# Kernel tuning notes

Hardware: AMD Instinct MI355X
Metric: run time of the kernel (lower is better)

The kernel has to match this reference:

```python
import jax, jax.numpy as jnp
import numpy as np
import math

H = 1024      # hidden_size
NH = 16       # num_heads
HD = H // NH  # head_dim
MS = 256      # memory_size
MD = 512      # memory_dim
B, S = 2, 2048


def setup_inputs() -> dict:
    key = jax.random.key(0)
    ks = jax.random.split(key, 12)
    sd = 1.0 / math.sqrt(H)
    inp = {
        "hidden_states": jax.random.normal(ks[0], (B, S, H), dtype=jnp.float32),
        "attention_mask": jnp.zeros((B, S), dtype=jnp.float32),
        "Wq": jax.random.normal(ks[1], (H, H), dtype=jnp.float32) * sd,
        "bq": jnp.zeros((H,), dtype=jnp.float32),
        "Wk": jax.random.normal(ks[2], (H, H), dtype=jnp.float32) * sd,
        "bk": jnp.zeros((H,), dtype=jnp.float32),
        "Wv": jax.random.normal(ks[3], (H, H), dtype=jnp.float32) * sd,
        "bv": jnp.zeros((H,), dtype=jnp.float32),
        "Wo": jax.random.normal(ks[4], (H, H), dtype=jnp.float32) * sd,
        "bo": jnp.zeros((H,), dtype=jnp.float32),
        "memory_values": jax.random.normal(ks[5], (MS, MD), dtype=jnp.float32),
        "Wmp": jax.random.normal(ks[6], (H, MD), dtype=jnp.float32) * (1.0 / math.sqrt(MD)),
        "bmp": jnp.zeros((H,), dtype=jnp.float32),
        "Wma": jax.random.normal(ks[7], (MS, H), dtype=jnp.float32) * sd,
        "bma": jnp.zeros((MS,), dtype=jnp.float32),
    }
    return inp


def reference(hidden_states, attention_mask, Wq, bq, Wk, bk, Wv, bv, Wo, bo,
              memory_values, Wmp, bmp, Wma, bma):
    b, s, h = hidden_states.shape
    scale = math.sqrt(HD)
    # projections (nn.Linear: x @ W.T + b)
    q = hidden_states @ Wq.T + bq
    k = hidden_states @ Wk.T + bk
    v = hidden_states @ Wv.T + bv
    # [b, nh, s, hd]
    q = q.reshape(b, s, NH, HD).transpose(0, 2, 1, 3)
    k = k.reshape(b, s, NH, HD).transpose(0, 2, 1, 3)
    v = v.reshape(b, s, NH, HD).transpose(0, 2, 1, 3)
    # full score matrix [b, nh, s, s] (faithful to original naive MHA)
    attn_scores = jnp.einsum('bhqd,bhkd->bhqk', q, k) / scale
    attn_scores = attn_scores + attention_mask[:, None, None, :] * (-1e9)
    attn_probs = jax.nn.softmax(attn_scores, axis=-1)  # dropout = identity (eval)
    attn_output = jnp.einsum('bhqk,bhkd->bhqd', attn_probs, v)
    attn_output = attn_output.transpose(0, 2, 1, 3).reshape(b, s, h)
    # memory-bank cross attention
    mem_scores = hidden_states @ Wma.T + bma            # [b, s, MS]
    mem_probs = jax.nn.softmax(mem_scores, axis=-1)
    mem_out = mem_probs @ memory_values                  # [b, s, MD]
    mem_out = mem_out @ Wmp.T + bmp                      # [b, s, H]
    combined = attn_output + 0.3 * mem_out
    return combined @ Wo.T + bo
```

## Files before the change

### kernel.cpp

```cpp
#include <hip/hip_runtime.h>

typedef __bf16 bf16;
typedef __bf16 bf16x8 __attribute__((ext_vector_type(8)));
typedef __bf16 bf16x4 __attribute__((ext_vector_type(4)));
typedef float  f32x4  __attribute__((ext_vector_type(4)));
typedef float  f32x16 __attribute__((ext_vector_type(16)));
typedef unsigned u32x2 __attribute__((ext_vector_type(2)));
typedef unsigned u32x4 __attribute__((ext_vector_type(4)));
typedef unsigned long long uptr;

#define MFMA16(a, b, c) __builtin_amdgcn_mfma_f32_16x16x32_bf16((a), (b), (c), 0, 0, 0)
#define MFMA32(a, b, c) __builtin_amdgcn_mfma_f32_32x32x16_bf16((a), (b), (c), 0, 0, 0)

__device__ __forceinline__ void gl_lds16(const void* g, void* l) {
  __builtin_amdgcn_global_load_lds(
      (__attribute__((address_space(1))) void*)(uptr)(g),
      (__attribute__((address_space(3))) void*)(uptr)(l),
      16, 0, 0);
}
__device__ __forceinline__ void gl_lds4(const void* g, void* l) {
  __builtin_amdgcn_global_load_lds(
      (__attribute__((address_space(1))) void*)(uptr)(g),
      (__attribute__((address_space(3))) void*)(uptr)(l),
      4, 0, 0);
}
__device__ __forceinline__ unsigned cvtpk_bf16(float lo, float hi) {
  unsigned r;
  asm("v_cvt_pk_bf16_f32 %0, %1, %2" : "=v"(r) : "v"(lo), "v"(hi));
  return r;
}

__global__ __launch_bounds__(256) void fused_prep(
    const float* __restrict__ X, const float* __restrict__ Wq,
    const float* __restrict__ Wk, const float* __restrict__ Wv,
    const float* __restrict__ Wo, const float* __restrict__ Wma,
    const float* __restrict__ Wmp, const float* __restrict__ mask,
    const float* __restrict__ bq, const float* __restrict__ bk,
    const float* __restrict__ bv, const float* __restrict__ mv,
    bf16* __restrict__ Xb, bf16* __restrict__ Wqkvb, bf16* __restrict__ Wob,
    bf16* __restrict__ Wmab, bf16* __restrict__ Wmpb,
    float* __restrict__ M2, float* __restrict__ bqkv, bf16* __restrict__ mvTb) {
  const int bid = blockIdx.x, t = threadIdx.x;
  auto cvt = [&](const float* src, bf16* dst, int blk) {
    const long i = ((long)blk * 256 + t) * 4;
    const float4 v = *(const float4*)(src + i);
    bf16x4 o = {(bf16)v.x, (bf16)v.y, (bf16)v.z, (bf16)v.w};
    *(bf16x4*)(dst + i) = o;
  };
  if (bid < 4096) cvt(X, Xb, bid);
  else if (bid < 5120) cvt(Wq, Wqkvb, bid - 4096);
  else if (bid < 6144) cvt(Wk, Wqkvb + 1024 * 1024, bid - 5120);
  else if (bid < 7168) cvt(Wv, Wqkvb + 2 * 1024 * 1024, bid - 6144);
  else if (bid < 8192) cvt(Wo, Wob, bid - 7168);
  else if (bid < 8448) cvt(Wma, Wmab, bid - 8192);
  else if (bid < 8960) cvt(Wmp, Wmpb, bid - 8448);
  else if (bid < 8964) {
    const long i = ((long)(bid - 8960) * 256 + t) * 4;
    const float4 v = *(const float4*)(mask + i);
    float4 o = {v.x * -1.44269504e9f, v.y * -1.44269504e9f,
                v.z * -1.44269504e9f, v.w * -1.44269504e9f};
    *(float4*)(M2 + i) = o;
  } else if (bid < 8967) {
    const int s = bid - 8964;
    const float* src = s == 0 ? bq : (s == 1 ? bk : bv);
    *(float4*)(bqkv + s * 1024 + t * 4) = *(const float4*)(src + t * 4);
  } else {
    const int d = bid - 8967;
    mvTb[(long)d * 256 + t] = (bf16)mv[(long)t * 512 + d];
  }
}

__global__ __launch_bounds__(256) void softmax_rows256(const float* __restrict__ in,
                                                       bf16* __restrict__ out) {
  const int w = threadIdx.x >> 6, l = threadIdx.x & 63;
  const long row = (long)blockIdx.x * 4 + w;
  const float4 v = *(const float4*)(in + row * 256 + l * 4);
  float mx = fmaxf(fmaxf(v.x, v.y), fmaxf(v.z, v.w));
  mx = fmaxf(mx, __shfl_xor(mx, 1, 64));
  mx = fmaxf(mx, __shfl_xor(mx, 2, 64));
  mx = fmaxf(mx, __shfl_xor(mx, 4, 64));
  mx = fmaxf(mx, __shfl_xor(mx, 8, 64));
  mx = fmaxf(mx, __shfl_xor(mx, 16, 64));
  mx = fmaxf(mx, __shfl_xor(mx, 32, 64));
  const float e0 = __expf(v.x - mx), e1 = __expf(v.y - mx);
  const float e2 = __expf(v.z - mx), e3 = __expf(v.w - mx);
  float sm = e0 + e1 + e2 + e3;
  sm += __shfl_xor(sm, 1, 64);
  sm += __shfl_xor(sm, 2, 64);
  sm += __shfl_xor(sm, 4, 64);
  sm += __shfl_xor(sm, 8, 64);
  sm += __shfl_xor(sm, 16, 64);
  sm += __shfl_xor(sm, 32, 64);
  const float inv = 1.0f / sm;
  bf16x4 o = {(bf16)(e0 * inv), (bf16)(e1 * inv), (bf16)(e2 * inv), (bf16)(e3 * inv)};
  *(bf16x4*)(out + row * 256 + l * 4) = o;
}

template <typename OutT, bool HAS_ADD>
__global__ __launch_bounds__(256, 3) void gemm_bt(
    const bf16* __restrict__ A, const bf16* __restrict__ B,
    const float* __restrict__ bias, const bf16* __restrict__ addsrc,
    OutT* __restrict__ C, int M, int N, int K, float alpha) {
  __shared__ bf16 lA[2][128 * 64];
  __shared__ bf16 lB[2][64 * 64];
  const int tid = threadIdx.x;
  const int w = tid >> 6, l = tid & 63;
  const int hi = l >> 4, lo = l & 15;
  const int m0 = blockIdx.y * 128, n0 = blockIdx.x * 64;
  const int wm = w * 32;

  const int sr8 = l >> 3;
  const int sc = (l & 7) * 8;
  const long aRow = (long)(m0 + wm + sr8);
  const long bRow = (long)(n0 + w * 16 + sr8);

  auto stage = [&](int p, int k0) {
#pragma unroll
    for (int j = 0; j < 4; ++j)
      gl_lds16(A + (aRow + 8 * j) * K + k0 + sc, (char*)lA[p] + (wm + 8 * j) * 128);
#pragma unroll
    for (int j = 0; j < 2; ++j)
      gl_lds16(B + (bRow + 8 * j) * K + k0 + sc, (char*)lB[p] + (w * 16 + 8 * j) * 128);
  };

  f32x4 acc[2][4] = {};
  stage(0, 0);
  __syncthreads();
  const int nt = K >> 6;

  for (int t = 0; t < nt; ++t) {
    const int p = t & 1;
    if (t + 1 < nt) stage(p ^ 1, (t + 1) << 6);
#pragma unroll
    for (int kk = 0; kk < 2; ++kk) {
      bf16x8 af[2], bfr[4];
#pragma unroll
      for (int mi = 0; mi < 2; ++mi)
        af[mi] = *(const bf16x8*)((const char*)lA[p] + (wm + mi * 16 + lo) * 128 + kk * 64 + hi * 16);
#pragma unroll
      for (int ni = 0; ni < 4; ++ni)
        bfr[ni] = *(const bf16x8*)((const char*)lB[p] + (ni * 16 + lo) * 128 + kk * 64 + hi * 16);
      __builtin_amdgcn_s_setprio(1);
#pragma unroll
      for (int mi = 0; mi < 2; ++mi)
#pragma unroll
        for (int ni = 0; ni < 4; ++ni)
          acc[mi][ni] = MFMA16(af[mi], bfr[ni], acc[mi][ni]);
      __builtin_amdgcn_s_setprio(0);
    }
    __syncthreads();
  }

#pragma unroll
  for (int ni = 0; ni < 4; ++ni) {
    const int col = n0 + ni * 16 + lo;
    const float bv = bias ? bias[col] : 0.0f;
#pragma unroll
    for (int mi = 0; mi < 2; ++mi) {
      const int mrow = m0 + wm + mi * 16 + hi * 4;
#pragma unroll
      for (int r = 0; r < 4; ++r) {
        const long row = mrow + r;
        float v = (acc[mi][ni][r] + bv) * alpha;
        if (HAS_ADD) v += (float)addsrc[row * N + col];
        C[row * (long)N + col] = (OutT)v;
      }
    }
  }
}

__global__ __launch_bounds__(256, 3) void gemm_qkv(
    const bf16* __restrict__ A, const bf16* __restrict__ B,
    const float* __restrict__ bias, bf16* __restrict__ Qo,
    bf16* __restrict__ Ko, bf16* __restrict__ Vto) {
  const int K = 1024;
  __shared__ bf16 lA[128 * 64];
  __shared__ bf16 lB[128 * 64];
  const int tid = threadIdx.x;
  const int w = tid >> 6, l = tid & 63;
  const int hi = l >> 4, lo = l & 15;
  const int m0 = blockIdx.y * 128, n0 = blockIdx.x * 128;
  const int wm = (w >> 1) * 64, wn = (w & 1) * 64;

  const int sr = w * 32 + (l >> 3);
  const int sc = (l & 7) * 8;
  const long aBase = (long)(m0 + sr) * K + sc;
  const long bBase = (long)(n0 + sr) * K + sc;

  f32x4 acc[4][4] = {};

  for (int k0 = 0; k0 < K; k0 += 64) {
#pragma unroll
    for (int j = 0; j < 4; ++j) {
      gl_lds16(A + aBase + (long)8 * j * K + k0, (char*)lA + (w * 32 + 8 * j) * 128);
      gl_lds16(B + bBase + (long)8 * j * K + k0, (char*)lB + (w * 32 + 8 * j) * 128);
    }
    __syncthreads();
#pragma unroll
    for (int kk = 0; kk < 2; ++kk) {
      bf16x8 af[4], bfr[4];
#pragma unroll
      for (int i = 0; i < 4; ++i) {
        af[i]  = *(const bf16x8*)((const char*)lA + (wm + i * 16 + lo) * 128 + kk * 64 + hi * 16);
        bfr[i] = *(const bf16x8*)((const char*)lB + (wn + i * 16 + lo) * 128 + kk * 64 + hi * 16);
      }
#pragma unroll
      for (int mi = 0; mi < 4; ++mi)
#pragma unroll
        for (int ni = 0; ni < 4; ++ni)
          acc[mi][ni] = MFMA16(af[mi], bfr[ni], acc[mi][ni]);
    }
    __syncthreads();
  }

  const int region = n0 >> 10;
#pragma unroll
  for (int ni = 0; ni < 4; ++ni) {
    const int col = n0 + wn + ni * 16 + lo;
    const float bv = bias[col];
#pragma unroll
    for (int mi = 0; mi < 4; ++mi) {
      const int mrow = m0 + wm + mi * 16 + hi * 4;
#pragma unroll
      for (int r = 0; r < 4; ++r) {
        const long row = mrow + r;
        const float v = acc[mi][ni][r] + bv;
        if (region == 0) {
          Qo[row * 1024 + col] = (bf16)v;
        } else if (region == 1) {
          Ko[row * 1024 + (col - 1024)] = (bf16)v;
        } else {
          const long bb = row >> 11, ss = row & 2047;
          Vto[(bb * 1024 + (col - 2048)) * 2048 + ss] = (bf16)v;
        }
      }
    }
  }
}

__global__ __launch_bounds__(256, 4) void attn_fwd(
    const bf16* __restrict__ Q, const bf16* __restrict__ Km,
    const bf16* __restrict__ Vt, const float* __restrict__ M2,
    bf16* __restrict__ Opart, float* __restrict__ ml) {
  __shared__ bf16 lK[2][64 * 64];
  __shared__ bf16 lV[2][64 * 64];
  __shared__ alignas(16) float lM[2][64];
  const int tid = threadIdx.x, w = tid >> 6, l = tid & 63;
  const int q31 = l & 31, h32 = l >> 5;
  const int b = blockIdx.z >> 1, half = blockIdx.z & 1;
  const int hh = blockIdx.y, q0 = blockIdx.x * 128;
  const long S = 2048, H = 1024;
  const int kbase = half * 1024;
  const float SCALE2 = 0.125f * 1.44269504f;

  bf16x8 qf[4];
  const long qrow = (long)b * S + q0 + w * 32 + q31;
#pragma unroll
  for (int sl = 0; sl < 4; ++sl)
    qf[sl] = *(const bf16x8*)(Q + qrow * H + hh * 64 + sl * 16 + h32 * 8);

  f32x16 o0 = {}, o1 = {};
  float mrun = -1e30f, lrun = 0.0f;

  const int swr = w * 16 + (l >> 3);
  const int swc = ((l & 7) ^ (l >> 3)) * 8;

  auto stage = [&](int p, int k0) {
#pragma unroll
    for (int j = 0; j < 2; ++j) {
      gl_lds16(Km + ((long)b * S + k0 + swr + 8 * j) * H + hh * 64 + swc,
               (char*)lK[p] + (w * 16 + 8 * j) * 128);
      gl_lds16(Vt + ((long)b * H + hh * 64 + swr + 8 * j) * S + k0 + swc,
               (char*)lV[p] + (w * 16 + 8 * j) * 128);
    }
    if (w == 0) gl_lds4(M2 + (long)b * S + k0 + l, (char*)lM[p]);
  };

  stage(0, kbase);
  __syncthreads();

  for (int t = 0; t < 16; ++t) {
    const int p = t & 1;
    if (t < 15) stage(p ^ 1, kbase + (t + 1) * 64);

    f32x16 s0 = {}, s1 = {};
    __builtin_amdgcn_s_setprio(1);
#pragma unroll
    for (int sl = 0; sl < 4; ++sl) {
      const int ch = sl * 2 + h32;
      const int cx = (ch ^ (q31 & 7)) * 16;
      const bf16x8 k0f = *(const bf16x8*)((const char*)lK[p] + q31 * 128 + cx);
      const bf16x8 k1f = *(const bf16x8*)((const char*)lK[p] + (32 + q31) * 128 + cx);
      s0 = MFMA32(k0f, qf[sl], s0);
      s1 = MFMA32(k1f, qf[sl], s1);
    }
    __builtin_amdgcn_s_setprio(0);

#pragma unroll
    for (int g = 0; g < 4; ++g) {
      const f32x4 m0 = *(const f32x4*)&lM[p][8 * g + 4 * h32];
      const f32x4 m1 = *(const f32x4*)&lM[p][32 + 8 * g + 4 * h32];
#pragma unroll
      for (int r = 0; r < 4; ++r) {
        s0[4 * g + r] = s0[4 * g + r] * SCALE2 + m0[r];
        s1[4 * g + r] = s1[4 * g + r] * SCALE2 + m1[r];
      }
    }

    f32x16 tm;
#pragma unroll
    for (int i = 0; i < 16; ++i) tm[i] = fmaxf(s0[i], s1[i]);
#pragma unroll
    for (int i = 0; i < 8; ++i) tm[i] = fmaxf(tm[i], tm[i + 8]);
#pragma unroll
    for (int i = 0; i < 4; ++i) tm[i] = fmaxf(tm[i], tm[i + 4]);
    float mx = fmaxf(fmaxf(tm[0], tm[1]), fmaxf(tm[2], tm[3]));
    mx = fmaxf(mx, __shfl_xor(mx, 32, 64));

    if (__any(mx > mrun + 8.0f)) {
      const float mn = fmaxf(mrun, mx);
      const float f = __builtin_amdgcn_exp2f(mrun - mn);
      mrun = mn;
      lrun *= f;
      float fb[16];
#pragma unroll
      for (int reg = 0; reg < 16; ++reg)
        fb[reg] = __shfl(f, (reg & 3) + 8 * (reg >> 2) + 4 * h32, 64);
#pragma unroll
      for (int reg = 0; reg < 16; ++reg) { o0[reg] *= fb[reg]; o1[reg] *= fb[reg]; }
    }

#pragma unroll
    for (int i = 0; i < 16; ++i) s0[i] = __builtin_amdgcn_exp2f(s0[i] - mrun);
#pragma unroll
    for (int i = 0; i < 16; ++i) s1[i] = __builtin_amdgcn_exp2f(s1[i] - mrun);

    f32x16 ts;
#pragma unroll
    for (int i = 0; i < 16; ++i) ts[i] = s0[i] + s1[i];
#pragma unroll
    for (int i = 0; i < 8; ++i) ts[i] += ts[i + 8];
#pragma unroll
    for (int i = 0; i < 4; ++i) ts[i] += ts[i + 4];
    float rs = (ts[0] + ts[1]) + (ts[2] + ts[3]);
    rs += __shfl_xor(rs, 32, 64);
    lrun += rs;

    bf16x8 pa[4];
#pragma unroll
    for (int ks = 0; ks < 4; ++ks) {
      const int rb = (ks & 1) * 8;
      unsigned a0, a1, b0, b1;
      if (ks < 2) {
        a0 = cvtpk_bf16(s0[rb + 0], s0[rb + 1]);
        a1 = cvtpk_bf16(s0[rb + 2], s0[rb + 3]);
        b0 = cvtpk_bf16(s0[rb + 4], s0[rb + 5]);
        b1 = cvtpk_bf16(s0[rb + 6], s0[rb + 7]);
      } else {
        a0 = cvtpk_bf16(s1[rb + 0], s1[rb + 1]);
        a1 = cvtpk_bf16(s1[rb + 2], s1[rb + 3]);
        b0 = cvtpk_bf16(s1[rb + 4], s1[rb + 5]);
        b1 = cvtpk_bf16(s1[rb + 6], s1[rb + 7]);
      }
      const u32x2 r02 = __builtin_amdgcn_permlane32_swap(a0, b0, false, false);
      const u32x2 r13 = __builtin_amdgcn_permlane32_swap(a1, b1, false, false);
      const u32x4 pw = {r02[0], r13[0], r02[1], r13[1]};
      pa[ks] = __builtin_bit_cast(bf16x8, pw);
    }

    __builtin_amdgcn_s_setprio(1);
#pragma unroll
    for (int ks = 0; ks < 4; ++ks) {
      const int ch = ks * 2 + h32;
      const int cx = (ch ^ (q31 & 7)) * 16;
      const bf16x8 v0 = *(const bf16x8*)((const char*)lV[p] + q31 * 128 + cx);
      const bf16x8 v1 = *(const bf16x8*)((const char*)lV[p] + (32 + q31) * 128 + cx);
      o0 = MFMA32(pa[ks], v0, o0);
      o1 = MFMA32(pa[ks], v1, o1);
    }
    __builtin_amdgcn_s_setprio(0);
    __syncthreads();
  }

  if (h32 == 0) {
    float2 v = {mrun, lrun};
    ((float2*)ml)[((long)half * 4096 + (long)b * 2048 + q0 + w * 32 + q31) * 16 + hh] = v;
  }
#pragma unroll
  for (int reg = 0; reg < 16; ++reg) {
    const int row = (reg & 3) + 8 * (reg >> 2) + 4 * h32;
    const long qg = (long)b * 2048 + q0 + w * 32 + row;
    Opart[((long)half * 4096 + qg) * 1024 + hh * 64 + q31]      = (bf16)o0[reg];
    Opart[((long)half * 4096 + qg) * 1024 + hh * 64 + 32 + q31] = (bf16)o1[reg];
  }
}

__global__ __launch_bounds__(256) void attn_combine(
    const bf16* __restrict__ Opart, const float* __restrict__ ml,
    bf16* __restrict__ AO) {
  const long i = ((long)blockIdx.x * 256 + threadIdx.x) * 4;
  const long qg = i >> 10;
  const int h = (int)((i & 1023) >> 6);
  const float2 a = ((const float2*)ml)[qg * 16 + h];
  const float2 c = ((const float2*)ml)[(4096 + qg) * 16 + h];
  const float m = fmaxf(a.x, c.x);
  const float w0 = __builtin_amdgcn_exp2f(a.x - m);
  const float w1 = __builtin_amdgcn_exp2f(c.x - m);
  const float inv = 1.0f / (w0 * a.y + w1 * c.y);
  const bf16x4 O0 = *(const bf16x4*)(Opart + i);
  const bf16x4 O1 = *(const bf16x4*)(Opart + 4096L * 1024 + i);
  bf16x4 o;
#pragma unroll
  for (int j = 0; j < 4; ++j)
    o[j] = (bf16)(((float)O0[j] * w0 + (float)O1[j] * w1) * inv);
  *(bf16x4*)(AO + i) = o;
}

extern "C" void kernel_launch(void* const* d_in, const int* in_sizes, int n_in,
                              void* d_out, int out_size, void* d_ws, size_t ws_size,
                              hipStream_t stream) {
  const float* X    = (const float*)d_in[0];
  const float* mask = (const float*)d_in[1];
  const float* Wq   = (const float*)d_in[2];  const float* bq  = (const float*)d_in[3];
  const float* Wk   = (const float*)d_in[4];  const float* bk  = (const float*)d_in[5];
  const float* Wv   = (const float*)d_in[6];  const float* bv  = (const float*)d_in[7];
  const float* Wo   = (const float*)d_in[8];  const float* bo  = (const float*)d_in[9];
  const float* mv   = (const float*)d_in[10];
  const float* Wmp  = (const float*)d_in[11]; const float* bmp = (const float*)d_in[12];
  const float* Wma  = (const float*)d_in[13]; const float* bma = (const float*)d_in[14];

  char* ws = (char*)d_ws;
  size_t off = 0;
  auto alloc = [&](size_t bytes) -> void* {
    void* p = ws + off;
    off += (bytes + 255) & ~(size_t)255;
    return p;
  };
  const long MS_ = 4096;
  bf16* Xb    = (bf16*)alloc(MS_ * 1024 * 2);
  bf16* Wqkvb = (bf16*)alloc(3072L * 1024 * 2);
  bf16* Wob   = (bf16*)alloc(1024 * 1024 * 2);
  bf16* Wmab  = (bf16*)alloc(256 * 1024 * 2);
  bf16* Wmpb  = (bf16*)alloc(1024 * 512 * 2);
  bf16* mvTb  = (bf16*)alloc(512 * 256 * 2);
  float* M2   = (float*)alloc(MS_ * 4);
  float* bqkv = (float*)alloc(3072 * 4);
  bf16* Qb    = (bf16*)alloc(MS_ * 1024 * 2);
  bf16* Kb    = (bf16*)alloc(MS_ * 1024 * 2);
  bf16* Vtb   = (bf16*)alloc(MS_ * 1024 * 2);
  bf16* AO    = (bf16*)alloc(MS_ * 1024 * 2);
  char* region = (char*)alloc(2 * MS_ * 1024 * 2 + MS_ * 16 * 8 + 1024);
  bf16* Opart = (bf16*)region;
  float* ml   = (float*)(region + 2 * MS_ * 1024 * 2);
  float* MSc  = (float*)region;
  bf16* MP    = (bf16*)(region + MS_ * 256 * 4);
  bf16* MO    = Kb;
  bf16* CB    = Qb;

  fused_prep<<<9479, 256, 0, stream>>>(X, Wq, Wk, Wv, Wo, Wma, Wmp, mask,
                                       bq, bk, bv, mv,
                                       Xb, Wqkvb, Wob, Wmab, Wmpb, M2, bqkv, mvTb);
  gemm_qkv<<<dim3(24, 32), 256, 0, stream>>>(Xb, Wqkvb, bqkv, Qb, Kb, Vtb);
  attn_fwd<<<dim3(16, 16, 4), 256, 0, stream>>>(Qb, Kb, Vtb, M2, Opart, ml);
  attn_combine<<<4096, 256, 0, stream>>>(Opart, ml, AO);
  gemm_bt<float, false><<<dim3(4, 32), 256, 0, stream>>>(Xb, Wmab, bma, nullptr, MSc, 4096, 256, 1024, 1.0f);
  softmax_rows256<<<1024, 256, 0, stream>>>(MSc, MP);
  gemm_bt<bf16, false><<<dim3(8, 32), 256, 0, stream>>>(MP, mvTb, nullptr, nullptr, MO, 4096, 512, 256, 1.0f);
  gemm_bt<bf16, true><<<dim3(16, 32), 256, 0, stream>>>(MO, Wmpb, bmp, AO, CB, 4096, 1024, 512, 0.3f);
  gemm_bt<float, false><<<dim3(16, 32), 256, 0, stream>>>(CB, Wob, bo, nullptr, (float*)d_out, 4096, 1024, 1024, 1.0f);
}
```

Baseline: 163.8 us.

## Fold memory projection into output weights and split attention keys into quarters

Precomputes Wo·(0.3·Wmp) as extra weight columns and a merged bias, so the memory projection GEMM with its residual add is dropped. The attention output and memory output are concatenated along K into one 1536-wide buffer for a single final GEMM. Attention is split into four key quarters with a remapped 1D grid and a higher occupancy target, the mask is read directly from global memory instead of LDS, and the combine step merges four partials. This adds a small weight-only GEMM, a per-call weight transpose, and an extra rounding of the folded weights to bf16.

```diff
diff --git a/kernel.cpp b/kernel.cpp
--- a/kernel.cpp
+++ b/kernel.cpp
@@ -18,12 +18,6 @@
       (__attribute__((address_space(3))) void*)(uptr)(l),
       16, 0, 0);
 }
-__device__ __forceinline__ void gl_lds4(const void* g, void* l) {
-  __builtin_amdgcn_global_load_lds(
-      (__attribute__((address_space(1))) void*)(uptr)(g),
-      (__attribute__((address_space(3))) void*)(uptr)(l),
-      4, 0, 0);
-}
 __device__ __forceinline__ unsigned cvtpk_bf16(float lo, float hi) {
   unsigned r;
   asm("v_cvt_pk_bf16_f32 %0, %1, %2" : "=v"(r) : "v"(lo), "v"(hi));
@@ -37,9 +31,11 @@
     const float* __restrict__ Wmp, const float* __restrict__ mask,
     const float* __restrict__ bq, const float* __restrict__ bk,
     const float* __restrict__ bv, const float* __restrict__ mv,
-    bf16* __restrict__ Xb, bf16* __restrict__ Wqkvb, bf16* __restrict__ Wob,
-    bf16* __restrict__ Wmab, bf16* __restrict__ Wmpb,
-    float* __restrict__ M2, float* __restrict__ bqkv, bf16* __restrict__ mvTb) {
+    const float* __restrict__ bo, const float* __restrict__ bmp,
+    bf16* __restrict__ Xb, bf16* __restrict__ Wqkvb, bf16* __restrict__ WCAT,
+    bf16* __restrict__ Wmab, bf16* __restrict__ WmpT,
+    float* __restrict__ M2, float* __restrict__ bqkv, bf16* __restrict__ mvTb,
+    float* __restrict__ bmix) {
   const int bid = blockIdx.x, t = threadIdx.x;
   auto cvt = [&](const float* src, bf16* dst, int blk) {
     const long i = ((long)blk * 256 + t) * 4;
@@ -51,10 +47,21 @@
   else if (bid < 5120) cvt(Wq, Wqkvb, bid - 4096);
   else if (bid < 6144) cvt(Wk, Wqkvb + 1024 * 1024, bid - 5120);
   else if (bid < 7168) cvt(Wv, Wqkvb + 2 * 1024 * 1024, bid - 6144);
-  else if (bid < 8192) cvt(Wo, Wob, bid - 7168);
-  else if (bid < 8448) cvt(Wma, Wmab, bid - 8192);
-  else if (bid < 8960) cvt(Wmp, Wmpb, bid - 8448);
-  else if (bid < 8964) {
+  else if (bid < 8192) {
+    const long i = ((long)(bid - 7168) * 256 + t) * 4;
+    const long row = i >> 10, col = i & 1023;
+    const float4 v = *(const float4*)(Wo + i);
+    bf16x4 o = {(bf16)v.x, (bf16)v.y, (bf16)v.z, (bf16)v.w};
+    *(bf16x4*)(WCAT + row * 1536 + col) = o;
+  } else if (bid < 8448) cvt(Wma, Wmab, bid - 8192);
+  else if (bid < 8960) {
+    const int m = bid - 8448;
+#pragma unroll
+    for (int j = 0; j < 4; ++j) {
+      const int k = t * 4 + j;
+      WmpT[(long)m * 1024 + k] = (bf16)Wmp[(long)k * 512 + m];
+    }
+  } else if (bid < 8964) {
     const long i = ((long)(bid - 8960) * 256 + t) * 4;
     const float4 v = *(const float4*)(mask + i);
     float4 o = {v.x * -1.44269504e9f, v.y * -1.44269504e9f,
@@ -64,9 +71,18 @@
     const int s = bid - 8964;
     const float* src = s == 0 ? bq : (s == 1 ? bk : bv);
     *(float4*)(bqkv + s * 1024 + t * 4) = *(const float4*)(src + t * 4);
-  } else {
+  } else if (bid < 9479) {
     const int d = bid - 8967;
     mvTb[(long)d * 256 + t] = (bf16)mv[(long)t * 512 + d];
+  } else {
+    const int n = (bid - 9479) * 256 + t;
+    float acc = 0.0f;
+    for (int k4 = 0; k4 < 256; ++k4) {
+      const float4 wv = *(const float4*)(Wo + (long)n * 1024 + k4 * 4);
+      const float4 bb = *(const float4*)(bmp + k4 * 4);
+      acc += wv.x * bb.x + wv.y * bb.y + wv.z * bb.z + wv.w * bb.w;
+    }
+    bmix[n] = bo[n] + 0.3f * acc;
   }
 }
 
@@ -96,11 +112,11 @@
   *(bf16x4*)(out + row * 256 + l * 4) = o;
 }
 
-template <typename OutT, bool HAS_ADD>
+template <typename OutT>
 __global__ __launch_bounds__(256, 3) void gemm_bt(
     const bf16* __restrict__ A, const bf16* __restrict__ B,
-    const float* __restrict__ bias, const bf16* __restrict__ addsrc,
-    OutT* __restrict__ C, int M, int N, int K, float alpha) {
+    const float* __restrict__ bias, OutT* __restrict__ C,
+    int M, int N, int K, int lda, int ldc, float alpha) {
   __shared__ bf16 lA[2][128 * 64];
   __shared__ bf16 lB[2][64 * 64];
   const int tid = threadIdx.x;
@@ -117,7 +133,7 @@
   auto stage = [&](int p, int k0) {
 #pragma unroll
     for (int j = 0; j < 4; ++j)
-      gl_lds16(A + (aRow + 8 * j) * K + k0 + sc, (char*)lA[p] + (wm + 8 * j) * 128);
+      gl_lds16(A + (aRow + 8 * j) * lda + k0 + sc, (char*)lA[p] + (wm + 8 * j) * 128);
 #pragma unroll
     for (int j = 0; j < 2; ++j)
       gl_lds16(B + (bRow + 8 * j) * K + k0 + sc, (char*)lB[p] + (w * 16 + 8 * j) * 128);
@@ -161,9 +177,7 @@
 #pragma unroll
       for (int r = 0; r < 4; ++r) {
         const long row = mrow + r;
-        float v = (acc[mi][ni][r] + bv) * alpha;
-        if (HAS_ADD) v += (float)addsrc[row * N + col];
-        C[row * (long)N + col] = (OutT)v;
+        C[row * (long)ldc + col] = (OutT)((acc[mi][ni][r] + bv) * alpha);
       }
     }
   }
@@ -238,19 +252,20 @@
   }
 }
 
-__global__ __launch_bounds__(256, 4) void attn_fwd(
+__global__ __launch_bounds__(256, 8) void attn_fwd(
     const bf16* __restrict__ Q, const bf16* __restrict__ Km,
     const bf16* __restrict__ Vt, const float* __restrict__ M2,
     bf16* __restrict__ Opart, float* __restrict__ ml) {
   __shared__ bf16 lK[2][64 * 64];
   __shared__ bf16 lV[2][64 * 64];
-  __shared__ alignas(16) float lM[2][64];
+  const int lin = blockIdx.x;
+  const int role = ((lin & 7) << 8) | (lin >> 3);
+  const int qt = role & 15, hh = (role >> 4) & 15, zz = role >> 8;
+  const int b = zz >> 2, quarter = zz & 3;
+  const int q0 = qt * 128, kbase = quarter * 512;
   const int tid = threadIdx.x, w = tid >> 6, l = tid & 63;
   const int q31 = l & 31, h32 = l >> 5;
-  const int b = blockIdx.z >> 1, half = blockIdx.z & 1;
-  const int hh = blockIdx.y, q0 = blockIdx.x * 128;
   const long S = 2048, H = 1024;
-  const int kbase = half * 1024;
   const float SCALE2 = 0.125f * 1.44269504f;
 
   bf16x8 qf[4];
@@ -273,15 +288,21 @@
       gl_lds16(Vt + ((long)b * H + hh * 64 + swr + 8 * j) * S + k0 + swc,
                (char*)lV[p] + (w * 16 + 8 * j) * 128);
     }
-    if (w == 0) gl_lds4(M2 + (long)b * S + k0 + l, (char*)lM[p]);
   };
 
   stage(0, kbase);
   __syncthreads();
 
-  for (int t = 0; t < 16; ++t) {
-    const int p = t & 1;
-    if (t < 15) stage(p ^ 1, kbase + (t + 1) * 64);
+  for (int t = 0; t < 8; ++t) {
+    const int p = t & 1, k0 = kbase + t * 64;
+    if (t < 7) stage(p ^ 1, k0 + 64);
+
+    f32x4 mk0[4], mk1[4];
+#pragma unroll
+    for (int g = 0; g < 4; ++g) {
+      mk0[g] = *(const f32x4*)(M2 + (long)b * S + k0 + 8 * g + 4 * h32);
+      mk1[g] = *(const f32x4*)(M2 + (long)b * S + k0 + 32 + 8 * g + 4 * h32);
+    }
 
     f32x16 s0 = {}, s1 = {};
     __builtin_amdgcn_s_setprio(1);
@@ -297,15 +318,12 @@
     __builtin_amdgcn_s_setprio(0);
 
 #pragma unroll
-    for (int g = 0; g < 4; ++g) {
-      const f32x4 m0 = *(const f32x4*)&lM[p][8 * g + 4 * h32];
-      const f32x4 m1 = *(const f32x4*)&lM[p][32 + 8 * g + 4 * h32];
+    for (int g = 0; g < 4; ++g)
 #pragma unroll
       for (int r = 0; r < 4; ++r) {
-        s0[4 * g + r] = s0[4 * g + r] * SCALE2 + m0[r];
-        s1[4 * g + r] = s1[4 * g + r] * SCALE2 + m1[r];
+        s0[4 * g + r] = s0[4 * g + r] * SCALE2 + mk0[g][r];
+        s1[4 * g + r] = s1[4 * g + r] * SCALE2 + mk1[g][r];
       }
-    }
 
     f32x16 tm;
 #pragma unroll
@@ -384,36 +402,43 @@
 
   if (h32 == 0) {
     float2 v = {mrun, lrun};
-    ((float2*)ml)[((long)half * 4096 + (long)b * 2048 + q0 + w * 32 + q31) * 16 + hh] = v;
+    ((float2*)ml)[((long)quarter * 4096 + (long)b * 2048 + q0 + w * 32 + q31) * 16 + hh] = v;
   }
 #pragma unroll
   for (int reg = 0; reg < 16; ++reg) {
     const int row = (reg & 3) + 8 * (reg >> 2) + 4 * h32;
     const long qg = (long)b * 2048 + q0 + w * 32 + row;
-    Opart[((long)half * 4096 + qg) * 1024 + hh * 64 + q31]      = (bf16)o0[reg];
-    Opart[((long)half * 4096 + qg) * 1024 + hh * 64 + 32 + q31] = (bf16)o1[reg];
+    Opart[((long)quarter * 4096 + qg) * 1024 + hh * 64 + q31]      = (bf16)o0[reg];
+    Opart[((long)quarter * 4096 + qg) * 1024 + hh * 64 + 32 + q31] = (bf16)o1[reg];
   }
 }
 
 __global__ __launch_bounds__(256) void attn_combine(
     const bf16* __restrict__ Opart, const float* __restrict__ ml,
-    bf16* __restrict__ AO) {
+    bf16* __restrict__ CAT) {
   const long i = ((long)blockIdx.x * 256 + threadIdx.x) * 4;
   const long qg = i >> 10;
   const int h = (int)((i & 1023) >> 6);
-  const float2 a = ((const float2*)ml)[qg * 16 + h];
-  const float2 c = ((const float2*)ml)[(4096 + qg) * 16 + h];
-  const float m = fmaxf(a.x, c.x);
-  const float w0 = __builtin_amdgcn_exp2f(a.x - m);
-  const float w1 = __builtin_amdgcn_exp2f(c.x - m);
-  const float inv = 1.0f / (w0 * a.y + w1 * c.y);
-  const bf16x4 O0 = *(const bf16x4*)(Opart + i);
-  const bf16x4 O1 = *(const bf16x4*)(Opart + 4096L * 1024 + i);
+  float2 a[4];
+#pragma unroll
+  for (int j = 0; j < 4; ++j) a[j] = ((const float2*)ml)[((long)j * 4096 + qg) * 16 + h];
+  const float m = fmaxf(fmaxf(a[0].x, a[1].x), fmaxf(a[2].x, a[3].x));
+  float wgt[4], den = 0.0f;
+#pragma unroll
+  for (int j = 0; j < 4; ++j) { wgt[j] = __builtin_amdgcn_exp2f(a[j].x - m); den += wgt[j] * a[j].y; }
+  const float inv = 1.0f / den;
+  float acc[4] = {};
+#pragma unroll
+  for (int j = 0; j < 4; ++j) {
+    const bf16x4 O = *(const bf16x4*)(Opart + (long)j * 4096 * 1024 + i);
+#pragma unroll
+    for (int e = 0; e < 4; ++e) acc[e] += (float)O[e] * wgt[j];
+  }
+  const long row = i >> 10, col = i & 1023;
   bf16x4 o;
 #pragma unroll
-  for (int j = 0; j < 4; ++j)
-    o[j] = (bf16)(((float)O0[j] * w0 + (float)O1[j] * w1) * inv);
-  *(bf16x4*)(AO + i) = o;
+  for (int e = 0; e < 4; ++e) o[e] = (bf16)(acc[e] * inv);
+  *(bf16x4*)(CAT + row * 1536 + col) = o;
 }
 
 extern "C" void kernel_launch(void* const* d_in, const int* in_sizes, int n_in,
@@ -439,33 +464,36 @@
   const long MS_ = 4096;
   bf16* Xb    = (bf16*)alloc(MS_ * 1024 * 2);
   bf16* Wqkvb = (bf16*)alloc(3072L * 1024 * 2);
-  bf16* Wob   = (bf16*)alloc(1024 * 1024 * 2);
+  bf16* WCAT  = (bf16*)alloc(1024L * 1536 * 2);
   bf16* Wmab  = (bf16*)alloc(256 * 1024 * 2);
-  bf16* Wmpb  = (bf16*)alloc(1024 * 512 * 2);
+  bf16* WmpT  = (bf16*)alloc(512L * 1024 * 2);
   bf16* mvTb  = (bf16*)alloc(512 * 256 * 2);
   float* M2   = (float*)alloc(MS_ * 4);
   float* bqkv = (float*)alloc(3072 * 4);
+  float* bmix = (float*)alloc(1024 * 4);
   bf16* Qb    = (bf16*)alloc(MS_ * 1024 * 2);
   bf16* Kb    = (bf16*)alloc(MS_ * 1024 * 2);
   bf16* Vtb   = (bf16*)alloc(MS_ * 1024 * 2);
-  bf16* AO    = (bf16*)alloc(MS_ * 1024 * 2);
-  char* region = (char*)alloc(2 * MS_ * 1024 * 2 + MS_ * 16 * 8 + 1024);
+  bf16* CAT   = (bf16*)alloc(MS_ * 1536 * 2);
+  char* region = (char*)alloc(4 * MS_ * 1024 * 2 + 4 * MS_ * 16 * 8 + 1024);
   bf16* Opart = (bf16*)region;
-  float* ml   = (float*)(region + 2 * MS_ * 1024 * 2);
+  float* ml   = (float*)(region + 4 * MS_ * 1024 * 2);
   float* MSc  = (float*)region;
   bf16* MP    = (bf16*)(region + MS_ * 256 * 4);
-  bf16* MO    = Kb;
-  bf16* CB    = Qb;
-
-  fused_prep<<<9479, 256, 0, stream>>>(X, Wq, Wk, Wv, Wo, Wma, Wmp, mask,
-                                       bq, bk, bv, mv,
-                                       Xb, Wqkvb, Wob, Wmab, Wmpb, M2, bqkv, mvTb);
+
+  fused_prep<<<9483, 256, 0, stream>>>(X, Wq, Wk, Wv, Wo, Wma, Wmp, mask,
+                                       bq, bk, bv, mv, bo, bmp,
+                                       Xb, Wqkvb, WCAT, Wmab, WmpT, M2, bqkv, mvTb, bmix);
+  gemm_bt<bf16><<<dim3(8, 8), 256, 0, stream>>>(WCAT, WmpT, nullptr, WCAT + 1024,
+                                                1024, 512, 1024, 1536, 1536, 0.3f);
   gemm_qkv<<<dim3(24, 32), 256, 0, stream>>>(Xb, Wqkvb, bqkv, Qb, Kb, Vtb);
-  attn_fwd<<<dim3(16, 16, 4), 256, 0, stream>>>(Qb, Kb, Vtb, M2, Opart, ml);
-  attn_combine<<<4096, 256, 0, stream>>>(Opart, ml, AO);
-  gemm_bt<float, false><<<dim3(4, 32), 256, 0, stream>>>(Xb, Wmab, bma, nullptr, MSc, 4096, 256, 1024, 1.0f);
+  attn_fwd<<<2048, 256, 0, stream>>>(Qb, Kb, Vtb, M2, Opart, ml);
+  attn_combine<<<4096, 256, 0, stream>>>(Opart, ml, CAT);
+  gemm_bt<float><<<dim3(4, 32), 256, 0, stream>>>(Xb, Wmab, bma, MSc,
+                                                  4096, 256, 1024, 1024, 256, 1.0f);
   softmax_rows256<<<1024, 256, 0, stream>>>(MSc, MP);
-  gemm_bt<bf16, false><<<dim3(8, 32), 256, 0, stream>>>(MP, mvTb, nullptr, nullptr, MO, 4096, 512, 256, 1.0f);
-  gemm_bt<bf16, true><<<dim3(16, 32), 256, 0, stream>>>(MO, Wmpb, bmp, AO, CB, 4096, 1024, 512, 0.3f);
-  gemm_bt<float, false><<<dim3(16, 32), 256, 0, stream>>>(CB, Wob, bo, nullptr, (float*)d_out, 4096, 1024, 1024, 1.0f);
-}
+  gemm_bt<bf16><<<dim3(8, 32), 256, 0, stream>>>(MP, mvTb, nullptr, CAT + 1024,
+                                                 4096, 512, 256, 256, 1536, 1.0f);
+  gemm_bt<float><<<dim3(16, 32), 256, 0, stream>>>(CAT, WCAT, bmix, (float*)d_out,
+                                                   4096, 1024, 1536, 1536, 1024, 1.0f);
+}
```

Measured after the change: 213.3 us. 1.3x slower.
